# Kernel tuning notes

Hardware: AMD Instinct MI355X
Metric: run time of the kernel (lower is better)

## Reference

```python
import jax, jax.numpy as jnp
import numpy as np

B, D, C = 8192, 2048, 1000
NUM_IDS = 256
MSEL_W, ORTH_W, CONS_W = 0.5, 0.1, 0.1


def setup_inputs() -> dict:
    key = jax.random.key(0)
    ks = jax.random.split(key, 7)
    return {
        "feat_shared": jax.random.normal(ks[0], (B, D), dtype=jnp.float32),
        "dee1": jax.random.normal(ks[1], (B, D), dtype=jnp.float32),
        "dee2": jax.random.normal(ks[2], (B, D), dtype=jnp.float32),
        "dee3": jax.random.normal(ks[3], (B, D), dtype=jnp.float32),
        "logits": jax.random.normal(ks[4], (B, C), dtype=jnp.float32),
        "labels": jax.random.randint(ks[5], (B,), 0, NUM_IDS, dtype=jnp.int32),
        "modal_ids": jax.random.randint(ks[6], (B,), 0, 2, dtype=jnp.int32),
    }


def _l2norm(x):
    return x / jnp.sqrt(jnp.sum(x * x, axis=1, keepdims=True)).clip(1e-12)


def _msel(features, labels, modal_ids):
    f = _l2norm(features)
    m_rgb = (modal_ids == 0).astype(f.dtype)  # [B]
    m_sar = (modal_ids == 1).astype(f.dtype)
    # per-label per-modal sums and counts via segment_sum (fixed NUM_IDS segments)
    sum_rgb = jax.ops.segment_sum(f * m_rgb[:, None], labels, num_segments=NUM_IDS)  # [L,D]
    sum_sar = jax.ops.segment_sum(f * m_sar[:, None], labels, num_segments=NUM_IDS)
    n_rgb = jax.ops.segment_sum(m_rgb, labels, num_segments=NUM_IDS)  # [L]
    n_sar = jax.ops.segment_sum(m_sar, labels, num_segments=NUM_IDS)
    c_rgb = sum_rgb / jnp.maximum(n_rgb, 1.0)[:, None]
    c_sar = sum_sar / jnp.maximum(n_sar, 1.0)[:, None]
    dist_cross = 1.0 - jnp.sum(c_rgb * c_sar, axis=1)
    # mean of Gram(f_rgb, f_rgb) == center_rgb . center_rgb (includes diagonal), same math
    dist_intra = 1.0 - jnp.sum(c_rgb * c_rgb, axis=1)
    valid = (n_rgb >= 2.0) & (n_sar >= 1.0)
    per_label = jnp.where(valid, (dist_cross - dist_intra) ** 2, 0.0)
    count = jnp.sum(valid.astype(f.dtype))
    return jnp.where(count > 0, jnp.sum(per_label) / jnp.maximum(count, 1.0), 0.0)


def _orth(f1, f2, f3):
    n1, n2, n3 = _l2norm(f1), _l2norm(f2), _l2norm(f3)
    s12 = jnp.mean(jnp.abs(jnp.sum(n1 * n2, axis=1)))
    s13 = jnp.mean(jnp.abs(jnp.sum(n1 * n3, axis=1)))
    s23 = jnp.mean(jnp.abs(jnp.sum(n2 * n3, axis=1)))
    return s12 + s13 + s23


def _consistency(logits, modal_ids):
    probs = jax.nn.softmax(logits, axis=1)  # [B,C]
    m_rgb = (modal_ids == 0).astype(probs.dtype)
    m_sar = (modal_ids == 1).astype(probs.dtype)
    n_rgb = jnp.sum(m_rgb)
    n_sar = jnp.sum(m_sar)
    p_rgb = jnp.sum(probs * m_rgb[:, None], axis=0) / jnp.maximum(n_rgb, 1.0)
    p_sar = jnp.sum(probs * m_sar[:, None], axis=0) / jnp.maximum(n_sar, 1.0)
    lr, ls = jnp.log(p_rgb), jnp.log(p_sar)
    # F.kl_div(log p, q, 'sum') = sum q*(log q - log p)
    kl = 0.5 * (jnp.sum(p_sar * (ls - lr)) + jnp.sum(p_rgb * (lr - ls)))
    return jnp.where((n_rgb > 0) & (n_sar > 0), kl, 0.0)


def reference(feat_shared, dee1, dee2, dee3, logits, labels, modal_ids):
    loss = MSEL_W * _msel(feat_shared, labels, modal_ids)
    loss = loss + ORTH_W * _orth(dee1, dee2, dee3)
    loss = loss + CONS_W * _consistency(logits, modal_ids)
    return loss
```

## Files before the change

kernel.cpp:

```cpp
#include <hip/hip_runtime.h>
#include <math.h>

#define B_   8192
#define D_   2048
#define C_   1000
#define L_   256
#define BIN_CAP 64

typedef unsigned short bf16raw;

__device__ __forceinline__ float bflo(unsigned int u) { return __uint_as_float(u << 16); }
__device__ __forceinline__ float bfhi(unsigned int u) { return __uint_as_float(u & 0xffff0000u); }

__device__ __forceinline__ bf16raw f2b(float f) {
  unsigned int x = __float_as_uint(f);
  unsigned int r = (x + 0x7fffu + ((x >> 16) & 1u)) >> 16;
  return (bf16raw)r;
}

__device__ __forceinline__ float waveSum(float v) {
#pragma unroll
  for (int off = 32; off > 0; off >>= 1) v += __shfl_xor(v, off, 64);
  return v;
}

__device__ __forceinline__ float waveMax(float v) {
#pragma unroll
  for (int off = 32; off > 0; off >>= 1) v = fmaxf(v, __shfl_xor(v, off, 64));
  return v;
}

__device__ __forceinline__ float blockSum(float v, float* lds4) {
  v = waveSum(v);
  const int wave = threadIdx.x >> 6;
  if ((threadIdx.x & 63) == 0) lds4[wave] = v;
  __syncthreads();
  v = lds4[0] + lds4[1] + lds4[2] + lds4[3];
  __syncthreads();
  return v;
}

template <int BF16>
__device__ __forceinline__ void load8(const void* p, size_t rowbase, int t, float* x) {
  if (BF16) {
    const uint4 v = ((const uint4*)((const bf16raw*)p + rowbase))[t];
    x[0] = bflo(v.x); x[1] = bfhi(v.x);
    x[2] = bflo(v.y); x[3] = bfhi(v.y);
    x[4] = bflo(v.z); x[5] = bfhi(v.z);
    x[6] = bflo(v.w); x[7] = bfhi(v.w);
  } else {
    const float4* q = (const float4*)((const float*)p + rowbase);
    const float4 v0 = q[2 * t], v1 = q[2 * t + 1];
    x[0] = v0.x; x[1] = v0.y; x[2] = v0.z; x[3] = v0.w;
    x[4] = v1.x; x[5] = v1.y; x[6] = v1.z; x[7] = v1.w;
  }
}

__global__ __launch_bounds__(256) void detect_kernel(const unsigned int* feat_words,
                                                     int* flag) {
  __shared__ float lds4[4];
  const unsigned int w = feat_words[threadIdx.x];
  const float v = bflo(w);
  const float a = fabsf(v);
  float hit = (a > 1e-3f && a < 10.f) ? 1.f : 0.f;
  hit = blockSum(hit, lds4);
  if (threadIdx.x == 0) *flag = (hit > 128.f) ? 1 : 0;
}

__global__ __launch_bounds__(256) void init_kernel(int* counts, float* accs,
                                                   float* p_final) {
  const int t = blockIdx.x * 256 + threadIdx.x;
  if (t < 2 * L_) counts[t] = 0;
  if (t < 16) accs[t] = 0.f;
  if (t < 2 * C_) p_final[t] = 0.f;
}

__global__ __launch_bounds__(256) void bin_kernel(const int* labels, const int* modal,
                                                  int* counts, int* rowlist) {
  const int r = blockIdx.x * 256 + threadIdx.x;
  if (r >= B_) return;
  const int m = modal[r] ? 1 : 0;
  int lb = labels[r]; lb = lb < 0 ? 0 : (lb >= L_ ? L_ - 1 : lb);
  const int key = m * L_ + lb;
  const int idx = atomicAdd(&counts[key], 1);
  if (idx < BIN_CAP) rowlist[key * BIN_CAP + idx] = r;
}

template <int BF16>
__global__ __launch_bounds__(256) void orth_kernel(const void* f1, const void* f2,
                                                   const void* f3, float* accs,
                                                   const int* flag) {
  if (*flag != BF16) return;
  __shared__ float lds[4][6];
  const int t = threadIdx.x;
  const int wave = t >> 6, lane = t & 63;
  float s12 = 0.f, s13 = 0.f, s23 = 0.f;
  for (int row = blockIdx.x; row < B_; row += gridDim.x) {
    const size_t base = (size_t)row * D_;
    float a[8], b[8], c[8];
    load8<BF16>(f1, base, t, a);
    load8<BF16>(f2, base, t, b);
    load8<BF16>(f3, base, t, c);
    float v[6] = {0.f, 0.f, 0.f, 0.f, 0.f, 0.f};
#pragma unroll
    for (int j = 0; j < 8; ++j) {
      v[0] += a[j] * a[j];
      v[1] += b[j] * b[j];
      v[2] += c[j] * c[j];
      v[3] += a[j] * b[j];
      v[4] += a[j] * c[j];
      v[5] += b[j] * c[j];
    }
#pragma unroll
    for (int j = 0; j < 6; ++j) v[j] = waveSum(v[j]);
    if (lane == 0) {
#pragma unroll
      for (int j = 0; j < 6; ++j) lds[wave][j] = v[j];
    }
    __syncthreads();
    if (t == 0) {
      float d[6];
#pragma unroll
      for (int j = 0; j < 6; ++j) d[j] = lds[0][j] + lds[1][j] + lds[2][j] + lds[3][j];
      const float q1 = fmaxf(sqrtf(d[0]), 1e-12f);
      const float q2 = fmaxf(sqrtf(d[1]), 1e-12f);
      const float q3 = fmaxf(sqrtf(d[2]), 1e-12f);
      s12 += fabsf(d[3]) / (q1 * q2);
      s13 += fabsf(d[4]) / (q1 * q3);
      s23 += fabsf(d[5]) / (q2 * q3);
    }
    __syncthreads();
  }
  if (t == 0) {
    atomicAdd(&accs[0], s12);
    atomicAdd(&accs[1], s13);
    atomicAdd(&accs[2], s23);
  }
}

template <int BF16>
__global__ __launch_bounds__(256) void label_kernel(const void* feat, const int* counts,
                                                    const int* rowlist, float* accs,
                                                    const int* flag) {
  if (*flag != BF16) return;
  __shared__ float lds4[4];
  const int l = blockIdx.x;
  const int t = threadIdx.x;
  const int nr_true = counts[l];
  const int ns_true = counts[L_ + l];
  const int nr = nr_true < BIN_CAP ? nr_true : BIN_CAP;
  const int ns = ns_true < BIN_CAP ? ns_true : BIN_CAP;
  float accR[8], accS[8];
#pragma unroll
  for (int j = 0; j < 8; ++j) { accR[j] = 0.f; accS[j] = 0.f; }
  for (int i = 0; i < nr + ns; ++i) {
    const int key = (i < nr) ? l : (L_ + l);
    const int idx = (i < nr) ? i : (i - nr);
    const int r = rowlist[key * BIN_CAP + idx];
    float x[8];
    load8<BF16>(feat, (size_t)r * D_, t, x);
    float ss = 0.f;
#pragma unroll
    for (int j = 0; j < 8; ++j) ss += x[j] * x[j];
    ss = blockSum(ss, lds4);
    const float rn = 1.f / fmaxf(sqrtf(ss), 1e-12f);
    if (i < nr) {
#pragma unroll
      for (int j = 0; j < 8; ++j) accR[j] += x[j] * rn;
    } else {
#pragma unroll
      for (int j = 0; j < 8; ++j) accS[j] += x[j] * rn;
    }
  }
  float rr = 0.f, rs = 0.f;
#pragma unroll
  for (int j = 0; j < 8; ++j) { rr += accR[j] * accR[j]; rs += accR[j] * accS[j]; }
  rr = blockSum(rr, lds4);
  rs = blockSum(rs, lds4);
  if (t == 0 && nr_true >= 2 && ns_true >= 1) {
    const float fr = (float)nr_true, fs = (float)ns_true;
    const float diff = rr / (fr * fr) - rs / (fr * fs);
    atomicAdd(&accs[3], diff * diff);
    atomicAdd(&accs[4], 1.0f);
  }
}

template <int BF16>
__global__ __launch_bounds__(256) void cons_kernel(const void* logits, const int* modal,
                                                   float* p_final, const int* flag) {
  if (*flag != BF16) return;
  __shared__ float wacc[4][2][1024];
  const int t = threadIdx.x;
  const int wave = t >> 6, lane = t & 63;
  float accA[16], accB[16];
#pragma unroll
  for (int k = 0; k < 16; ++k) { accA[k] = 0.f; accB[k] = 0.f; }
  const int rbase = blockIdx.x * 32 + wave * 8;
  for (int i = 0; i < 8; ++i) {
    const int r = rbase + i;
    float x[16];
#pragma unroll
    for (int kk = 0; kk < 4; ++kk) {
      const int idx = lane + (kk << 6);
      if (idx < (C_ / 4)) {
        if (BF16) {
          const uint2 w = ((const uint2*)((const bf16raw*)logits + (size_t)r * C_))[idx];
          x[4 * kk + 0] = bflo(w.x); x[4 * kk + 1] = bfhi(w.x);
          x[4 * kk + 2] = bflo(w.y); x[4 * kk + 3] = bfhi(w.y);
        } else {
          const float4 w = ((const float4*)((const float*)logits + (size_t)r * C_))[idx];
          x[4 * kk + 0] = w.x; x[4 * kk + 1] = w.y;
          x[4 * kk + 2] = w.z; x[4 * kk + 3] = w.w;
        }
      } else {
        x[4 * kk + 0] = -INFINITY; x[4 * kk + 1] = -INFINITY;
        x[4 * kk + 2] = -INFINITY; x[4 * kk + 3] = -INFINITY;
      }
    }
    float mx = -INFINITY;
#pragma unroll
    for (int k = 0; k < 16; ++k) mx = fmaxf(mx, x[k]);
    mx = waveMax(mx);
    float s = 0.f;
#pragma unroll
    for (int k = 0; k < 16; ++k) {
      x[k] = expf(x[k] - mx);
      s += x[k];
    }
    s = waveSum(s);
    const float inv = 1.f / s;
    if (modal[r] == 0) {
#pragma unroll
      for (int k = 0; k < 16; ++k) accA[k] += x[k] * inv;
    } else {
#pragma unroll
      for (int k = 0; k < 16; ++k) accB[k] += x[k] * inv;
    }
  }
#pragma unroll
  for (int k = 0; k < 16; ++k) {
    const int c = 4 * (lane + ((k >> 2) << 6)) + (k & 3);
    wacc[wave][0][c] = accA[k];
    wacc[wave][1][c] = accB[k];
  }
  __syncthreads();
  for (int e = t; e < 2 * C_; e += 256) {
    const int m = (e < C_) ? 0 : 1;
    const int c = e - m * C_;
    atomicAdd(&p_final[e], wacc[0][m][c] + wacc[1][m][c] + wacc[2][m][c] + wacc[3][m][c]);
  }
}

__global__ __launch_bounds__(256) void InnovationLoss_88124138979690_kernel(
    const float* p_final, const int* counts, const float* accs, void* out,
    const int* flag) {
  __shared__ float lds4[4];
  const int t = threadIdx.x;
  const float nr = blockSum((float)counts[t], lds4);
  const float ns = blockSum((float)counts[L_ + t], lds4);
  const float fr = fmaxf(nr, 1.f), fs = fmaxf(ns, 1.f);
  float klp = 0.f;
  for (int c = t; c < C_; c += 256) {
    const float pr = p_final[c] / fr;
    const float ps = p_final[C_ + c] / fs;
    klp += (ps - pr) * (logf(ps) - logf(pr));
  }
  klp = blockSum(klp, lds4);
  if (t == 0) {
    const float kl = (nr > 0.f && ns > 0.f) ? 0.5f * klp : 0.f;
    const float msel_cnt = accs[4];
    const float msel = msel_cnt > 0.f ? accs[3] / fmaxf(msel_cnt, 1.f) : 0.f;
    const float orth = (accs[0] + accs[1] + accs[2]) * (1.0f / (float)B_);
    const float res = 0.5f * msel + 0.1f * orth + 0.1f * kl;
    if (*flag) ((bf16raw*)out)[0] = f2b(res);
    else       ((float*)out)[0]   = res;
  }
}

extern "C" __attribute__((visibility("default")))
void kernel_launch(void* const* d_in, const int* in_sizes, int n_in,
                   void* d_out, int out_size, void* d_ws, size_t ws_size,
                   hipStream_t stream) {
  const void* feat   = d_in[0];
  const void* dee1   = d_in[1];
  const void* dee2   = d_in[2];
  const void* dee3   = d_in[3];
  const void* logits = d_in[4];
  const int*  labels = (const int*)d_in[5];
  const int*  modal  = (const int*)d_in[6];

  char* ws = (char*)d_ws;
  int*   counts  = (int*)  (ws);
  float* accs    = (float*)(ws + 2048);
  float* p_final = (float*)(ws + 2112);
  int*   rowlist = (int*)  (ws + 10112);
  int*   flag    = (int*)  (ws + 141184);

  detect_kernel<<<1, 256, 0, stream>>>((const unsigned int*)feat, flag);
  init_kernel<<<8, 256, 0, stream>>>(counts, accs, p_final);
  bin_kernel<<<B_ / 256, 256, 0, stream>>>(labels, modal, counts, rowlist);
  cons_kernel<1><<<B_ / 32, 256, 0, stream>>>(logits, modal, p_final, flag);
  cons_kernel<0><<<B_ / 32, 256, 0, stream>>>(logits, modal, p_final, flag);
  orth_kernel<1><<<2048, 256, 0, stream>>>(dee1, dee2, dee3, accs, flag);
  orth_kernel<0><<<2048, 256, 0, stream>>>(dee1, dee2, dee3, accs, flag);
  label_kernel<1><<<L_, 256, 0, stream>>>(feat, counts, rowlist, accs, flag);
  label_kernel<0><<<L_, 256, 0, stream>>>(feat, counts, rowlist, accs, flag);
  InnovationLoss_88124138979690_kernel<<<1, 256, 0, stream>>>(p_final, counts, accs,
                                                              d_out, flag);
}
```

Baseline: 372.9 us.

## Merge orth and feature-norm passes into wave-per-row kernel, drop dtype template duplicates

Replaces the templated dual-launch kernels with single runtime-dtype kernels. A new rowdot kernel handles one row per wave (no block barriers per row) for the orthogonality dots and also computes per-row inverse norms of feat, which the label kernel now reuses instead of doing a block reduction per gathered row. Orth partials are written per block and reduced in the final kernel instead of via atomics. The softmax and label loops process two rows per iteration for more memory-level parallelism, at the cost of extra register pressure and one more full read of feat.

```diff
diff --git a/kernel.cpp b/kernel.cpp
--- a/kernel.cpp
+++ b/kernel.cpp
@@ -6,6 +6,7 @@
 #define C_   1000
 #define L_   256
 #define BIN_CAP 64
+#define ORTH_BLOCKS 2048
 
 typedef unsigned short bf16raw;
 
@@ -18,15 +19,16 @@
   return (bf16raw)r;
 }
 
+__device__ __forceinline__ void dec8(uint4 u, float* x) {
+  x[0] = bflo(u.x); x[1] = bfhi(u.x);
+  x[2] = bflo(u.y); x[3] = bfhi(u.y);
+  x[4] = bflo(u.z); x[5] = bfhi(u.z);
+  x[6] = bflo(u.w); x[7] = bfhi(u.w);
+}
+
 __device__ __forceinline__ float waveSum(float v) {
 #pragma unroll
   for (int off = 32; off > 0; off >>= 1) v += __shfl_xor(v, off, 64);
-  return v;
-}
-
-__device__ __forceinline__ float waveMax(float v) {
-#pragma unroll
-  for (int off = 32; off > 0; off >>= 1) v = fmaxf(v, __shfl_xor(v, off, 64));
   return v;
 }
 
@@ -40,14 +42,11 @@
   return v;
 }
 
-template <int BF16>
-__device__ __forceinline__ void load8(const void* p, size_t rowbase, int t, float* x) {
-  if (BF16) {
+__device__ __forceinline__ void load8rt(const void* p, size_t rowbase, int t, int isb,
+                                        float* x) {
+  if (isb) {
     const uint4 v = ((const uint4*)((const bf16raw*)p + rowbase))[t];
-    x[0] = bflo(v.x); x[1] = bfhi(v.x);
-    x[2] = bflo(v.y); x[3] = bfhi(v.y);
-    x[4] = bflo(v.z); x[5] = bfhi(v.z);
-    x[6] = bflo(v.w); x[7] = bfhi(v.w);
+    dec8(v, x);
   } else {
     const float4* q = (const float4*)((const float*)p + rowbase);
     const float4 v0 = q[2 * t], v1 = q[2 * t + 1];
@@ -86,90 +85,241 @@
   if (idx < BIN_CAP) rowlist[key * BIN_CAP + idx] = r;
 }
 
-template <int BF16>
-__global__ __launch_bounds__(256) void orth_kernel(const void* f1, const void* f2,
-                                                   const void* f3, float* accs,
-                                                   const int* flag) {
-  if (*flag != BF16) return;
-  __shared__ float lds[4][6];
+__global__ __launch_bounds__(256) void rowdot_kernel(const void* f1, const void* f2,
+                                                     const void* f3, const void* feat,
+                                                     float* orth_part, float* norms,
+                                                     const int* flag) {
+  __shared__ float lsum[4][3];
   const int t = threadIdx.x;
   const int wave = t >> 6, lane = t & 63;
-  float s12 = 0.f, s13 = 0.f, s23 = 0.f;
-  for (int row = blockIdx.x; row < B_; row += gridDim.x) {
+  const int isb = *flag;
+
+  if (blockIdx.x < ORTH_BLOCKS) {
+    const int row = blockIdx.x * 4 + wave;
     const size_t base = (size_t)row * D_;
-    float a[8], b[8], c[8];
-    load8<BF16>(f1, base, t, a);
-    load8<BF16>(f2, base, t, b);
-    load8<BF16>(f3, base, t, c);
     float v[6] = {0.f, 0.f, 0.f, 0.f, 0.f, 0.f};
-#pragma unroll
-    for (int j = 0; j < 8; ++j) {
-      v[0] += a[j] * a[j];
-      v[1] += b[j] * b[j];
-      v[2] += c[j] * c[j];
-      v[3] += a[j] * b[j];
-      v[4] += a[j] * c[j];
-      v[5] += b[j] * c[j];
-    }
-#pragma unroll
-    for (int j = 0; j < 6; ++j) v[j] = waveSum(v[j]);
+    if (isb) {
+      const uint4* qa = (const uint4*)((const bf16raw*)f1 + base);
+      const uint4* qb = (const uint4*)((const bf16raw*)f2 + base);
+      const uint4* qc = (const uint4*)((const bf16raw*)f3 + base);
+      uint4 A[4], Bv[4], Cv[4];
+#pragma unroll
+      for (int j = 0; j < 4; ++j) A[j] = qa[j * 64 + lane];
+#pragma unroll
+      for (int j = 0; j < 4; ++j) Bv[j] = qb[j * 64 + lane];
+#pragma unroll
+      for (int j = 0; j < 4; ++j) Cv[j] = qc[j * 64 + lane];
+#pragma unroll
+      for (int j = 0; j < 4; ++j) {
+        float a[8], b[8], c[8];
+        dec8(A[j], a); dec8(Bv[j], b); dec8(Cv[j], c);
+#pragma unroll
+        for (int k = 0; k < 8; ++k) {
+          v[0] += a[k] * a[k]; v[1] += b[k] * b[k]; v[2] += c[k] * c[k];
+          v[3] += a[k] * b[k]; v[4] += a[k] * c[k]; v[5] += b[k] * c[k];
+        }
+      }
+    } else {
+      const float4* qa = (const float4*)((const float*)f1 + base);
+      const float4* qb = (const float4*)((const float*)f2 + base);
+      const float4* qc = (const float4*)((const float*)f3 + base);
+#pragma unroll
+      for (int h = 0; h < 2; ++h) {
+        float4 A[4], Bv[4], Cv[4];
+#pragma unroll
+        for (int j = 0; j < 4; ++j) A[j] = qa[(h * 4 + j) * 64 + lane];
+#pragma unroll
+        for (int j = 0; j < 4; ++j) Bv[j] = qb[(h * 4 + j) * 64 + lane];
+#pragma unroll
+        for (int j = 0; j < 4; ++j) Cv[j] = qc[(h * 4 + j) * 64 + lane];
+#pragma unroll
+        for (int j = 0; j < 4; ++j) {
+          const float a[4] = {A[j].x, A[j].y, A[j].z, A[j].w};
+          const float b[4] = {Bv[j].x, Bv[j].y, Bv[j].z, Bv[j].w};
+          const float c[4] = {Cv[j].x, Cv[j].y, Cv[j].z, Cv[j].w};
+#pragma unroll
+          for (int k = 0; k < 4; ++k) {
+            v[0] += a[k] * a[k]; v[1] += b[k] * b[k]; v[2] += c[k] * c[k];
+            v[3] += a[k] * b[k]; v[4] += a[k] * c[k]; v[5] += b[k] * c[k];
+          }
+        }
+      }
+    }
+#pragma unroll
+    for (int off = 32; off > 0; off >>= 1) {
+#pragma unroll
+      for (int j = 0; j < 6; ++j) v[j] += __shfl_xor(v[j], off, 64);
+    }
+    const float q1 = fmaxf(sqrtf(v[0]), 1e-12f);
+    const float q2 = fmaxf(sqrtf(v[1]), 1e-12f);
+    const float q3 = fmaxf(sqrtf(v[2]), 1e-12f);
     if (lane == 0) {
-#pragma unroll
-      for (int j = 0; j < 6; ++j) lds[wave][j] = v[j];
+      lsum[wave][0] = fabsf(v[3]) / (q1 * q2);
+      lsum[wave][1] = fabsf(v[4]) / (q1 * q3);
+      lsum[wave][2] = fabsf(v[5]) / (q2 * q3);
     }
     __syncthreads();
-    if (t == 0) {
-      float d[6];
-#pragma unroll
-      for (int j = 0; j < 6; ++j) d[j] = lds[0][j] + lds[1][j] + lds[2][j] + lds[3][j];
-      const float q1 = fmaxf(sqrtf(d[0]), 1e-12f);
-      const float q2 = fmaxf(sqrtf(d[1]), 1e-12f);
-      const float q3 = fmaxf(sqrtf(d[2]), 1e-12f);
-      s12 += fabsf(d[3]) / (q1 * q2);
-      s13 += fabsf(d[4]) / (q1 * q3);
-      s23 += fabsf(d[5]) / (q2 * q3);
-    }
-    __syncthreads();
-  }
-  if (t == 0) {
-    atomicAdd(&accs[0], s12);
-    atomicAdd(&accs[1], s13);
-    atomicAdd(&accs[2], s23);
-  }
-}
-
-template <int BF16>
+    if (t < 3) {
+      orth_part[t * ORTH_BLOCKS + blockIdx.x] =
+          lsum[0][t] + lsum[1][t] + lsum[2][t] + lsum[3][t];
+    }
+  } else {
+    const int row = (blockIdx.x - ORTH_BLOCKS) * 4 + wave;
+    const size_t base = (size_t)row * D_;
+    float ss = 0.f;
+    if (isb) {
+      const uint4* q = (const uint4*)((const bf16raw*)feat + base);
+      uint4 X[4];
+#pragma unroll
+      for (int j = 0; j < 4; ++j) X[j] = q[j * 64 + lane];
+#pragma unroll
+      for (int j = 0; j < 4; ++j) {
+        float x[8]; dec8(X[j], x);
+#pragma unroll
+        for (int k = 0; k < 8; ++k) ss += x[k] * x[k];
+      }
+    } else {
+      const float4* q = (const float4*)((const float*)feat + base);
+#pragma unroll
+      for (int j = 0; j < 8; ++j) {
+        const float4 w = q[j * 64 + lane];
+        ss += w.x * w.x + w.y * w.y + w.z * w.z + w.w * w.w;
+      }
+    }
+    ss = waveSum(ss);
+    if (lane == 0) norms[row] = 1.f / fmaxf(sqrtf(ss), 1e-12f);
+  }
+}
+
+__device__ __forceinline__ void loadlogits(const void* logits, int r, int lane, int isb,
+                                           float* x) {
+#pragma unroll
+  for (int kk = 0; kk < 4; ++kk) {
+    const int idx = lane + (kk << 6);
+    if (idx < (C_ / 4)) {
+      if (isb) {
+        const uint2 w = ((const uint2*)((const bf16raw*)logits + (size_t)r * C_))[idx];
+        x[4 * kk + 0] = bflo(w.x); x[4 * kk + 1] = bfhi(w.x);
+        x[4 * kk + 2] = bflo(w.y); x[4 * kk + 3] = bfhi(w.y);
+      } else {
+        const float4 w = ((const float4*)((const float*)logits + (size_t)r * C_))[idx];
+        x[4 * kk + 0] = w.x; x[4 * kk + 1] = w.y;
+        x[4 * kk + 2] = w.z; x[4 * kk + 3] = w.w;
+      }
+    } else {
+      x[4 * kk + 0] = -INFINITY; x[4 * kk + 1] = -INFINITY;
+      x[4 * kk + 2] = -INFINITY; x[4 * kk + 3] = -INFINITY;
+    }
+  }
+}
+
+__global__ __launch_bounds__(256) void cons_kernel(const void* logits, const int* modal,
+                                                   float* p_final, const int* flag) {
+  __shared__ float wacc[4][2][1024];
+  const int t = threadIdx.x;
+  const int wave = t >> 6, lane = t & 63;
+  const int isb = *flag;
+  float accA[16], accB[16];
+#pragma unroll
+  for (int k = 0; k < 16; ++k) { accA[k] = 0.f; accB[k] = 0.f; }
+  const int rbase = blockIdx.x * 32 + wave * 8;
+#pragma unroll
+  for (int i = 0; i < 8; i += 2) {
+    const int r0 = rbase + i, r1 = rbase + i + 1;
+    float x[16], y[16];
+    loadlogits(logits, r0, lane, isb, x);
+    loadlogits(logits, r1, lane, isb, y);
+    float mx = -INFINITY, my = -INFINITY;
+#pragma unroll
+    for (int k = 0; k < 16; ++k) { mx = fmaxf(mx, x[k]); my = fmaxf(my, y[k]); }
+#pragma unroll
+    for (int off = 32; off > 0; off >>= 1) {
+      mx = fmaxf(mx, __shfl_xor(mx, off, 64));
+      my = fmaxf(my, __shfl_xor(my, off, 64));
+    }
+    float sx = 0.f, sy = 0.f;
+#pragma unroll
+    for (int k = 0; k < 16; ++k) {
+      x[k] = expf(x[k] - mx); sx += x[k];
+      y[k] = expf(y[k] - my); sy += y[k];
+    }
+#pragma unroll
+    for (int off = 32; off > 0; off >>= 1) {
+      sx += __shfl_xor(sx, off, 64);
+      sy += __shfl_xor(sy, off, 64);
+    }
+    const float ivx = 1.f / sx, ivy = 1.f / sy;
+    if (modal[r0] == 0) {
+#pragma unroll
+      for (int k = 0; k < 16; ++k) accA[k] += x[k] * ivx;
+    } else {
+#pragma unroll
+      for (int k = 0; k < 16; ++k) accB[k] += x[k] * ivx;
+    }
+    if (modal[r1] == 0) {
+#pragma unroll
+      for (int k = 0; k < 16; ++k) accA[k] += y[k] * ivy;
+    } else {
+#pragma unroll
+      for (int k = 0; k < 16; ++k) accB[k] += y[k] * ivy;
+    }
+  }
+#pragma unroll
+  for (int k = 0; k < 16; ++k) {
+    const int c = 4 * (lane + ((k >> 2) << 6)) + (k & 3);
+    wacc[wave][0][c] = accA[k];
+    wacc[wave][1][c] = accB[k];
+  }
+  __syncthreads();
+  for (int e = t; e < 2 * C_; e += 256) {
+    const int m = (e < C_) ? 0 : 1;
+    const int c = e - m * C_;
+    atomicAdd(&p_final[e], wacc[0][m][c] + wacc[1][m][c] + wacc[2][m][c] + wacc[3][m][c]);
+  }
+}
+
 __global__ __launch_bounds__(256) void label_kernel(const void* feat, const int* counts,
-                                                    const int* rowlist, float* accs,
-                                                    const int* flag) {
-  if (*flag != BF16) return;
+                                                    const int* rowlist, const float* norms,
+                                                    float* accs, const int* flag) {
   __shared__ float lds4[4];
   const int l = blockIdx.x;
   const int t = threadIdx.x;
+  const int isb = *flag;
   const int nr_true = counts[l];
   const int ns_true = counts[L_ + l];
   const int nr = nr_true < BIN_CAP ? nr_true : BIN_CAP;
   const int ns = ns_true < BIN_CAP ? ns_true : BIN_CAP;
+  const int tot = nr + ns;
   float accR[8], accS[8];
 #pragma unroll
   for (int j = 0; j < 8; ++j) { accR[j] = 0.f; accS[j] = 0.f; }
-  for (int i = 0; i < nr + ns; ++i) {
-    const int key = (i < nr) ? l : (L_ + l);
-    const int idx = (i < nr) ? i : (i - nr);
-    const int r = rowlist[key * BIN_CAP + idx];
-    float x[8];
-    load8<BF16>(feat, (size_t)r * D_, t, x);
-    float ss = 0.f;
-#pragma unroll
-    for (int j = 0; j < 8; ++j) ss += x[j] * x[j];
-    ss = blockSum(ss, lds4);
-    const float rn = 1.f / fmaxf(sqrtf(ss), 1e-12f);
+  for (int i = 0; i < tot; i += 2) {
+    const int i1 = i + 1;
+    const int key0 = (i < nr) ? l : (L_ + l);
+    const int idx0 = (i < nr) ? i : (i - nr);
+    const int r0 = rowlist[key0 * BIN_CAP + idx0];
+    const bool have1 = (i1 < tot);
+    const int key1 = (i1 < nr) ? l : (L_ + l);
+    const int idx1 = (i1 < nr) ? i1 : (i1 - nr);
+    const int r1 = have1 ? rowlist[key1 * BIN_CAP + idx1] : r0;
+    const float rn0 = norms[r0];
+    const float rn1 = have1 ? norms[r1] : 0.f;
+    float x0[8], x1[8];
+    load8rt(feat, (size_t)r0 * D_, t, isb, x0);
+    load8rt(feat, (size_t)r1 * D_, t, isb, x1);
     if (i < nr) {
 #pragma unroll
-      for (int j = 0; j < 8; ++j) accR[j] += x[j] * rn;
-    } else {
-#pragma unroll
-      for (int j = 0; j < 8; ++j) accS[j] += x[j] * rn;
+      for (int j = 0; j < 8; ++j) accR[j] += x0[j] * rn0;
+    } else {
+#pragma unroll
+      for (int j = 0; j < 8; ++j) accS[j] += x0[j] * rn0;
+    }
+    if (i1 < nr) {
+#pragma unroll
+      for (int j = 0; j < 8; ++j) accR[j] += x1[j] * rn1;
+    } else {
+#pragma unroll
+      for (int j = 0; j < 8; ++j) accS[j] += x1[j] * rn1;
     }
   }
   float rr = 0.f, rs = 0.f;
@@ -185,75 +335,9 @@
   }
 }
 
-template <int BF16>
-__global__ __launch_bounds__(256) void cons_kernel(const void* logits, const int* modal,
-                                                   float* p_final, const int* flag) {
-  if (*flag != BF16) return;
-  __shared__ float wacc[4][2][1024];
-  const int t = threadIdx.x;
-  const int wave = t >> 6, lane = t & 63;
-  float accA[16], accB[16];
-#pragma unroll
-  for (int k = 0; k < 16; ++k) { accA[k] = 0.f; accB[k] = 0.f; }
-  const int rbase = blockIdx.x * 32 + wave * 8;
-  for (int i = 0; i < 8; ++i) {
-    const int r = rbase + i;
-    float x[16];
-#pragma unroll
-    for (int kk = 0; kk < 4; ++kk) {
-      const int idx = lane + (kk << 6);
-      if (idx < (C_ / 4)) {
-        if (BF16) {
-          const uint2 w = ((const uint2*)((const bf16raw*)logits + (size_t)r * C_))[idx];
-          x[4 * kk + 0] = bflo(w.x); x[4 * kk + 1] = bfhi(w.x);
-          x[4 * kk + 2] = bflo(w.y); x[4 * kk + 3] = bfhi(w.y);
-        } else {
-          const float4 w = ((const float4*)((const float*)logits + (size_t)r * C_))[idx];
-          x[4 * kk + 0] = w.x; x[4 * kk + 1] = w.y;
-          x[4 * kk + 2] = w.z; x[4 * kk + 3] = w.w;
-        }
-      } else {
-        x[4 * kk + 0] = -INFINITY; x[4 * kk + 1] = -INFINITY;
-        x[4 * kk + 2] = -INFINITY; x[4 * kk + 3] = -INFINITY;
-      }
-    }
-    float mx = -INFINITY;
-#pragma unroll
-    for (int k = 0; k < 16; ++k) mx = fmaxf(mx, x[k]);
-    mx = waveMax(mx);
-    float s = 0.f;
-#pragma unroll
-    for (int k = 0; k < 16; ++k) {
-      x[k] = expf(x[k] - mx);
-      s += x[k];
-    }
-    s = waveSum(s);
-    const float inv = 1.f / s;
-    if (modal[r] == 0) {
-#pragma unroll
-      for (int k = 0; k < 16; ++k) accA[k] += x[k] * inv;
-    } else {
-#pragma unroll
-      for (int k = 0; k < 16; ++k) accB[k] += x[k] * inv;
-    }
-  }
-#pragma unroll
-  for (int k = 0; k < 16; ++k) {
-    const int c = 4 * (lane + ((k >> 2) << 6)) + (k & 3);
-    wacc[wave][0][c] = accA[k];
-    wacc[wave][1][c] = accB[k];
-  }
-  __syncthreads();
-  for (int e = t; e < 2 * C_; e += 256) {
-    const int m = (e < C_) ? 0 : 1;
-    const int c = e - m * C_;
-    atomicAdd(&p_final[e], wacc[0][m][c] + wacc[1][m][c] + wacc[2][m][c] + wacc[3][m][c]);
-  }
-}
-
 __global__ __launch_bounds__(256) void InnovationLoss_88124138979690_kernel(
-    const float* p_final, const int* counts, const float* accs, void* out,
-    const int* flag) {
+    const float* p_final, const int* counts, const float* accs, const float* orth_part,
+    void* out, const int* flag) {
   __shared__ float lds4[4];
   const int t = threadIdx.x;
   const float nr = blockSum((float)counts[t], lds4);
@@ -266,11 +350,20 @@
     klp += (ps - pr) * (logf(ps) - logf(pr));
   }
   klp = blockSum(klp, lds4);
+  float o0 = 0.f, o1 = 0.f, o2 = 0.f;
+  for (int b = t; b < ORTH_BLOCKS; b += 256) {
+    o0 += orth_part[b];
+    o1 += orth_part[ORTH_BLOCKS + b];
+    o2 += orth_part[2 * ORTH_BLOCKS + b];
+  }
+  o0 = blockSum(o0, lds4);
+  o1 = blockSum(o1, lds4);
+  o2 = blockSum(o2, lds4);
   if (t == 0) {
     const float kl = (nr > 0.f && ns > 0.f) ? 0.5f * klp : 0.f;
     const float msel_cnt = accs[4];
     const float msel = msel_cnt > 0.f ? accs[3] / fmaxf(msel_cnt, 1.f) : 0.f;
-    const float orth = (accs[0] + accs[1] + accs[2]) * (1.0f / (float)B_);
+    const float orth = (o0 + o1 + o2) * (1.0f / (float)B_);
     const float res = 0.5f * msel + 0.1f * orth + 0.1f * kl;
     if (*flag) ((bf16raw*)out)[0] = f2b(res);
     else       ((float*)out)[0]   = res;
@@ -290,21 +383,21 @@
   const int*  modal  = (const int*)d_in[6];
 
   char* ws = (char*)d_ws;
-  int*   counts  = (int*)  (ws);
-  float* accs    = (float*)(ws + 2048);
-  float* p_final = (float*)(ws + 2112);
-  int*   rowlist = (int*)  (ws + 10112);
-  int*   flag    = (int*)  (ws + 141184);
+  int*   counts    = (int*)  (ws);
+  float* accs      = (float*)(ws + 2048);
+  float* p_final   = (float*)(ws + 2112);
+  int*   rowlist   = (int*)  (ws + 10112);
+  int*   flag      = (int*)  (ws + 141184);
+  float* norms     = (float*)(ws + 141248);
+  float* orth_part = (float*)(ws + 174016);
 
   detect_kernel<<<1, 256, 0, stream>>>((const unsigned int*)feat, flag);
   init_kernel<<<8, 256, 0, stream>>>(counts, accs, p_final);
   bin_kernel<<<B_ / 256, 256, 0, stream>>>(labels, modal, counts, rowlist);
-  cons_kernel<1><<<B_ / 32, 256, 0, stream>>>(logits, modal, p_final, flag);
-  cons_kernel<0><<<B_ / 32, 256, 0, stream>>>(logits, modal, p_final, flag);
-  orth_kernel<1><<<2048, 256, 0, stream>>>(dee1, dee2, dee3, accs, flag);
-  orth_kernel<0><<<2048, 256, 0, stream>>>(dee1, dee2, dee3, accs, flag);
-  label_kernel<1><<<L_, 256, 0, stream>>>(feat, counts, rowlist, accs, flag);
-  label_kernel<0><<<L_, 256, 0, stream>>>(feat, counts, rowlist, accs, flag);
+  rowdot_kernel<<<2 * ORTH_BLOCKS, 256, 0, stream>>>(dee1, dee2, dee3, feat, orth_part,
+                                                     norms, flag);
+  cons_kernel<<<B_ / 32, 256, 0, stream>>>(logits, modal, p_final, flag);
+  label_kernel<<<L_, 256, 0, stream>>>(feat, counts, rowlist, norms, accs, flag);
   InnovationLoss_88124138979690_kernel<<<1, 256, 0, stream>>>(p_final, counts, accs,
-                                                              d_out, flag);
-}
+                                                              orth_part, d_out, flag);
+}
```

Measured after the change: 316.2 us. 15.2% less time.
